# Kernel optimization log

Hardware: AMD Instinct MI355X
Metric: run time of the kernel (lower is better)

## Reference

```python
import jax, jax.numpy as jnp
import numpy as np

NB = 8            # num_blocks
D = 128           # embed_dim
D_INNER = 256     # expand=2
HEADS = 4
P = 64            # headdim
N = 32            # d_state
K = 4             # d_conv
CONV_DIM = D_INNER + 2 * N          # 320 (x, B, C streams)
D_IN_PROJ = 2 * D_INNER + 2 * N + HEADS  # 580 (z, xBC, dt)


def setup_inputs():
    key = jax.random.key(0)
    ks = iter(jax.random.split(key, 16))
    f = lambda shape, s=0.02: (jax.random.normal(next(ks), shape, jnp.float32) * s)
    B, L = 2, 4096
    return {
        'x': jax.random.normal(next(ks), (B, L, D), jnp.float32),
        'residual': jnp.zeros((B, L, D), jnp.float32),
        'ln1_w': jnp.ones((NB, D)), 'ln1_b': jnp.zeros((NB, D)),
        'ln2_w': jnp.ones((NB, D)), 'ln2_b': jnp.zeros((NB, D)),
        'fc1_w': f((NB, 4 * D, D)), 'fc1_b': jnp.zeros((NB, 4 * D)),
        'fc2_w': f((NB, D, 2 * D)), 'fc2_b': jnp.zeros((NB, D)),
        'in_proj_w': f((NB, D_IN_PROJ, D)),
        'conv_w': f((NB, CONV_DIM, K), 0.1), 'conv_b': jnp.zeros((NB, CONV_DIM)),
        'dt_bias': f((NB, HEADS), 0.1),
        'A_log': jnp.tile(jnp.log(jnp.arange(1, HEADS + 1, dtype=jnp.float32)), (NB, 1)),
        'Dp': jnp.ones((NB, HEADS)),
        'rms_w': jnp.ones((NB, D_INNER)),
        'out_proj_w': f((NB, D, D_INNER)),
        'h': 64, 'w': 64,
    }


def layernorm(x, w, b):
    mu = jnp.mean(x, -1, keepdims=True)
    var = jnp.mean((x - mu) ** 2, -1, keepdims=True)
    return (x - mu) * jax.lax.rsqrt(var + 1e-5) * w + b


def mamba2(x, in_proj_w, conv_w, conv_b, dt_bias, A_log, Dp, rms_w, out_proj_w):
    Bb, L, _ = x.shape
    zxbcdt = jnp.einsum('bld,ed->ble', x, in_proj_w)          # [B,L,580]
    z = zxbcdt[..., :D_INNER]
    xBC = zxbcdt[..., D_INNER:D_INNER + CONV_DIM]
    dt = jax.nn.softplus(zxbcdt[..., -HEADS:] + dt_bias)      # [B,L,H]
    # causal depthwise conv1d + silu
    xc = jnp.moveaxis(xBC, 1, 2)                              # [B,C,L]
    xc = jax.lax.conv_general_dilated(xc, conv_w[:, None, :], (1,), [(K - 1, 0)],
                                      feature_group_count=CONV_DIM)
    xBC = jax.nn.silu(jnp.moveaxis(xc, 1, 2) + conv_b)
    xs = xBC[..., :D_INNER].reshape(Bb, L, HEADS, P)          # [B,L,H,P]
    Bm = xBC[..., D_INNER:D_INNER + N]                        # [B,L,N]
    Cm = xBC[..., D_INNER + N:]                               # [B,L,N]
    dA = jnp.exp(dt * (-jnp.exp(A_log)))                      # [B,L,H]

    def step(hst, inp):
        dA_t, dt_t, B_t, C_t, x_t = inp
        hst = hst * dA_t[:, :, None, None] + (dt_t[:, :, None, None] * x_t[..., None]) * B_t[:, None, None, :]
        return hst, jnp.einsum('bhpn,bn->bhp', hst, C_t)

    tfirst = lambda a: jnp.moveaxis(a, 1, 0)
    h0 = jnp.zeros((Bb, HEADS, P, N), x.dtype)
    _, ys = jax.lax.scan(step, h0, (tfirst(dA), tfirst(dt), tfirst(Bm), tfirst(Cm), tfirst(xs)))
    y = jnp.moveaxis(ys, 0, 1) + Dp[None, None, :, None] * xs # [B,L,H,P]
    y = y.reshape(Bb, L, D_INNER) * jax.nn.silu(z)            # gated
    y = y * jax.lax.rsqrt(jnp.mean(y * y, -1, keepdims=True) + 1e-5) * rms_w
    return jnp.einsum('be,de->bd'.replace('b', 'bl'), y, out_proj_w)


def mlp(x, fc1_w, fc1_b, fc2_w, fc2_b):
    x12 = jnp.einsum('bld,ed->ble', x, fc1_w) + fc1_b
    x1, x2 = jnp.split(x12, 2, axis=-1)
    return jnp.einsum('ble,de->bld', jax.nn.silu(x1) * x2, fc2_w) + fc2_b


def reference(x, residual, ln1_w, ln1_b, ln2_w, ln2_b, fc1_w, fc1_b, fc2_w, fc2_b,
              in_proj_w, conv_w, conv_b, dt_bias, A_log, Dp, rms_w, out_proj_w, h, w):
    for i in range(NB):
        residual = x
        x1 = layernorm(residual, ln1_w[i], ln1_b[i])
        x_m = residual + mamba2(x1, in_proj_w[i], conv_w[i], conv_b[i], dt_bias[i],
                                A_log[i], Dp[i], rms_w[i], out_proj_w[i])
        residual = x_m
        x2 = layernorm(residual, ln2_w[i], ln2_b[i])
        x = residual + mlp(x2, fc1_w[i], fc1_b[i], fc2_w[i], fc2_b[i])
    return (x, residual)
```

## Files before the change

kernel.cpp:

```cpp
#include <hip/hip_runtime.h>
#include <hip/hip_bf16.h>
#include <cstddef>

#define NBLK 8
#define DD   128
#define DI   256
#define NH   4
#define PP   64
#define NNs  32
#define EE   580
#define BB   2
#define LLEN 4096
#define ML   (BB*LLEN)
#define SEGS 256
#define TT   16
#define GPAD 264

typedef unsigned short u16;
typedef short bf16x8 __attribute__((ext_vector_type(8)));
typedef float f32x4 __attribute__((ext_vector_type(4)));

__device__ __forceinline__ float siluf(float x){ return x / (1.f + expf(-x)); }
__device__ __forceinline__ float b2f(u16 u){ return __uint_as_float((unsigned)u << 16); }
__device__ __forceinline__ u16 f2b(float f){
    __hip_bfloat16 h = __float2bfloat16(f);
    return *reinterpret_cast<u16*>(&h);
}
__device__ __forceinline__ void ld8f(const u16* p, float* f){
    ushort4 a = *(const ushort4*)p;
    ushort4 b = *(const ushort4*)(p + 4);
    f[0]=b2f(a.x); f[1]=b2f(a.y); f[2]=b2f(a.z); f[3]=b2f(a.w);
    f[4]=b2f(b.x); f[5]=b2f(b.y); f[6]=b2f(b.z); f[7]=b2f(b.w);
}

#define IPW_N (NBLK*EE*DD)
#define OPW_N (NBLK*DD*DI)
#define F1W_N (NBLK*512*DD)
#define F2W_N (NBLK*DD*DI)
#define CVT_TOT (IPW_N+OPW_N+F1W_N+F2W_N)

__global__ __launch_bounds__(256) void cvt_weights(const float* __restrict__ ip,
                                                   const float* __restrict__ op,
                                                   const float* __restrict__ f1,
                                                   const float* __restrict__ f2,
                                                   const float* __restrict__ xin,
                                                   u16* __restrict__ dip,
                                                   u16* __restrict__ dop,
                                                   u16* __restrict__ df1,
                                                   u16* __restrict__ df2,
                                                   float* __restrict__ xout)
{
    int i = blockIdx.x * 256 + threadIdx.x;
    if (i < IPW_N)                          dip[i] = f2b(ip[i]);
    else if (i < IPW_N + OPW_N)             dop[i - IPW_N] = f2b(op[i - IPW_N]);
    else if (i < IPW_N + OPW_N + F1W_N)     df1[i - IPW_N - OPW_N] = f2b(f1[i - IPW_N - OPW_N]);
    else                                    df2[i - IPW_N - OPW_N - F1W_N] = f2b(f2[i - IPW_N - OPW_N - F1W_N]);
    if (i < ML * DD) xout[i] = xin[i];
}

__global__ __launch_bounds__(256) void inproj_ln_gemm(const float* __restrict__ X,
                                                      const float* __restrict__ lnw,
                                                      const float* __restrict__ lnb,
                                                      const u16* __restrict__ W,
                                                      u16* __restrict__ C)
{
    __shared__ __align__(16) u16 Ash[64*128];
    __shared__ __align__(16) u16 Wsh[64*128];
    __shared__ float red[64][8];
    const int tid = threadIdx.x;
    const int wave = tid >> 6, lane = tid & 63;
    const int l15 = lane & 15, quad = lane >> 4;
    const int bm = blockIdx.y * 64;
    const int lrow = tid >> 2, sub = tid & 3;

    const float* xr = X + (size_t)(bm + lrow) * DD + sub*32;
    float4 xv[8];
    float ps = 0.f, pq = 0.f;
#pragma unroll
    for (int i = 0; i < 8; i++) {
        xv[i] = *(const float4*)(xr + i*4);
        ps += xv[i].x + xv[i].y + xv[i].z + xv[i].w;
        pq += xv[i].x*xv[i].x + xv[i].y*xv[i].y + xv[i].z*xv[i].z + xv[i].w*xv[i].w;
    }
    red[lrow][sub] = ps; red[lrow][4+sub] = pq;
    __syncthreads();
    float s = red[lrow][0]+red[lrow][1]+red[lrow][2]+red[lrow][3];
    float q = red[lrow][4]+red[lrow][5]+red[lrow][6]+red[lrow][7];
    float mu = s * (1.f/DD);
    float rstd = rsqrtf(q*(1.f/DD) - mu*mu + 1e-5f);
#pragma unroll
    for (int i = 0; i < 4; i++) {
        float4 a0 = xv[2*i], a1 = xv[2*i+1];
        int c0 = sub*32 + i*8;
        u16 o[8];
        o[0] = f2b((a0.x-mu)*rstd*lnw[c0+0] + lnb[c0+0]);
        o[1] = f2b((a0.y-mu)*rstd*lnw[c0+1] + lnb[c0+1]);
        o[2] = f2b((a0.z-mu)*rstd*lnw[c0+2] + lnb[c0+2]);
        o[3] = f2b((a0.w-mu)*rstd*lnw[c0+3] + lnb[c0+3]);
        o[4] = f2b((a1.x-mu)*rstd*lnw[c0+4] + lnb[c0+4]);
        o[5] = f2b((a1.y-mu)*rstd*lnw[c0+5] + lnb[c0+5]);
        o[6] = f2b((a1.z-mu)*rstd*lnw[c0+6] + lnb[c0+6]);
        o[7] = f2b((a1.w-mu)*rstd*lnw[c0+7] + lnb[c0+7]);
        *(uint4*)&Ash[((size_t)(sub*4+i)*64 + lrow) * 8] = *(uint4*)o;
    }

#pragma unroll 1
    for (int t2 = 0; t2 < 2; t2++) {
        int bn = (blockIdx.x * 2 + t2) * 64;
        __syncthreads();
#pragma unroll
        for (int i = 0; i < 4; i++) {
            int k8 = sub + 4*i;
            uint4 wv = make_uint4(0u,0u,0u,0u);
            if (bn + lrow < EE)
                wv = *(const uint4*)(W + (size_t)(bn + lrow) * DD + k8*8);
            *(uint4*)&Wsh[((size_t)k8*64 + lrow) * 8] = wv;
        }
        __syncthreads();

        f32x4 acc[4];
#pragma unroll
        for (int nt = 0; nt < 4; nt++) acc[nt] = (f32x4){0.f,0.f,0.f,0.f};
#pragma unroll
        for (int kk = 0; kk < 4; kk++) {
            bf16x8 af = *(const bf16x8*)&Ash[(((kk*4 + quad)*64) + wave*16 + l15) * 8];
#pragma unroll
            for (int nt = 0; nt < 4; nt++) {
                bf16x8 bfv = *(const bf16x8*)&Wsh[(((kk*4 + quad)*64) + nt*16 + l15) * 8];
                acc[nt] = __builtin_amdgcn_mfma_f32_16x16x32_bf16(af, bfv, acc[nt], 0, 0, 0);
            }
        }
#pragma unroll
        for (int nt = 0; nt < 4; nt++) {
            int n = bn + nt*16 + l15;
            if (n < EE) {
#pragma unroll
                for (int r = 0; r < 4; r++) {
                    int m = bm + wave*16 + quad*4 + r;
                    C[(size_t)m * EE + n] = f2b(acc[nt][r]);
                }
            }
        }
    }
}

__global__ __launch_bounds__(256) void scan1(const u16* __restrict__ zx,
                                             const float* __restrict__ cw,
                                             const float* __restrict__ cb,
                                             const float* __restrict__ dt_bias,
                                             const float* __restrict__ A_log,
                                             u16* __restrict__ seg,
                                             float* __restrict__ segsum)
{
    __shared__ float Bsh[4][TT*NNs];
    __shared__ float dts[4][TT], das[4][TT];
    int wv = threadIdx.x >> 6;
    int p = threadIdx.x & 63;
    int sg = blockIdx.x % (SEGS/4);
    int bh = blockIdx.x / (SEGS/4);
    int h = bh % NH;
    int b = bh / NH;
    int s = sg*4 + wv;
    int l0 = s * TT;
    int row0 = b * LLEN + l0;

    float xr[TT+3];
    const u16* xcol = zx + (size_t)row0 * EE + 256 + h*64 + p;
#pragma unroll
    for (int r = 0; r < TT+3; r++) {
        int l = l0 - 3 + r;
        xr[r] = (l >= 0) ? b2f(xcol[(ptrdiff_t)(r-3) * EE]) : 0.f;
    }
    float4 wx = *(const float4*)(cw + (size_t)(h*64+p) * 4);
    float cbx = cb[h*64+p];

    if (p < NNs) {
        float br[TT+3];
        const u16* bcol = zx + (size_t)row0 * EE + 512 + p;
#pragma unroll
        for (int r = 0; r < TT+3; r++) {
            int l = l0 - 3 + r;
            br[r] = (l >= 0) ? b2f(bcol[(ptrdiff_t)(r-3) * EE]) : 0.f;
        }
        float4 wb = *(const float4*)(cw + (size_t)(256+p) * 4);
        float cbb = cb[256+p];
#pragma unroll
        for (int t = 0; t < TT; t++)
            Bsh[wv][t*NNs + p] = siluf(cbb + wb.x*br[t] + wb.y*br[t+1] + wb.z*br[t+2] + wb.w*br[t+3]);
    }
    if (p < TT) {
        float v = b2f(zx[(size_t)(row0+p)*EE + (EE-NH) + h]) + dt_bias[h];
        float dt = (v > 20.f) ? v : log1pf(expf(v));
        dts[wv][p] = dt;
        das[wv][p] = expf(-expf(A_log[h]) * dt);
    }
    __syncthreads();

    float hreg[NNs];
#pragma unroll
    for (int n = 0; n < NNs; n++) hreg[n] = 0.f;
    float sdt = 0.f;
#pragma unroll
    for (int t = 0; t < TT; t++) {
        float dA = das[wv][t];
        float dt = dts[wv][t];
        float xv = siluf(cbx + wx.x*xr[t] + wx.y*xr[t+1] + wx.z*xr[t+2] + wx.w*xr[t+3]);
        float dtx = dt * xv;
#pragma unroll
        for (int n4 = 0; n4 < 8; n4++) {
            float4 Bv = *(const float4*)&Bsh[wv][t*NNs + n4*4];
            hreg[n4*4+0] = fmaf(hreg[n4*4+0], dA, dtx * Bv.x);
            hreg[n4*4+1] = fmaf(hreg[n4*4+1], dA, dtx * Bv.y);
            hreg[n4*4+2] = fmaf(hreg[n4*4+2], dA, dtx * Bv.z);
            hreg[n4*4+3] = fmaf(hreg[n4*4+3], dA, dtx * Bv.w);
        }
        sdt += dt;
    }
    int bidg = bh * SEGS + s;
    u16* dst = seg + ((size_t)bidg * PP + p) * NNs;
#pragma unroll
    for (int n8 = 0; n8 < 4; n8++) {
        u16 ob[8];
#pragma unroll
        for (int j = 0; j < 8; j++) ob[j] = f2b(hreg[n8*8 + j]);
        *(uint4*)(dst + n8*8) = *(uint4*)ob;
    }
    if (p == 0) segsum[bidg] = sdt;
}

__global__ __launch_bounds__(256) void scan2(u16* __restrict__ seg,
                                             const float* __restrict__ segsum,
                                             const float* __restrict__ A_log)
{
    int bh = blockIdx.x >> 3;
    int chunk = blockIdx.x & 7;
    int h = bh % NH;
    int entry = chunk * 256 + threadIdx.x;
    float negA = -expf(A_log[h]);
    float hs = 0.f;
    const float* ss = segsum + bh * SEGS;
    u16* base = seg + (size_t)bh * SEGS * (PP * NNs) + entry;
    for (int j0 = 0; j0 < SEGS; j0 += 16) {
        float e[16], a[16];
#pragma unroll
        for (int k = 0; k < 16; k++) {
            a[k] = ss[j0 + k];
            e[k] = b2f(base[(size_t)(j0 + k) * (PP * NNs)]);
        }
#pragma unroll
        for (int k = 0; k < 16; k++) {
            float Aj = expf(negA * a[k]);
            base[(size_t)(j0 + k) * (PP * NNs)] = f2b(hs);
            hs = fmaf(Aj, hs, e[k]);
        }
    }
}

__global__ __launch_bounds__(256) void scan3(const u16* __restrict__ zx,
                                             const float* __restrict__ cw,
                                             const float* __restrict__ cb,
                                             const float* __restrict__ dt_bias,
                                             const float* __restrict__ A_log,
                                             const u16* __restrict__ seg,
                                             const float* __restrict__ Dp,
                                             u16* __restrict__ y)
{
    __shared__ float BCsh[4][TT*64];
    __shared__ float dts[4][TT], das[4][TT];
    int wv = threadIdx.x >> 6;
    int p = threadIdx.x & 63;
    int sg = blockIdx.x % (SEGS/4);
    int bh = blockIdx.x / (SEGS/4);
    int h = bh % NH;
    int b = bh / NH;
    int s = sg*4 + wv;
    int l0 = s * TT;
    int row0 = b * LLEN + l0;

    float xr[TT+3];
    const u16* xcol = zx + (size_t)row0 * EE + 256 + h*64 + p;
#pragma unroll
    for (int r = 0; r < TT+3; r++) {
        int l = l0 - 3 + r;
        xr[r] = (l >= 0) ? b2f(xcol[(ptrdiff_t)(r-3) * EE]) : 0.f;
    }
    float4 wx = *(const float4*)(cw + (size_t)(h*64+p) * 4);
    float cbx = cb[h*64+p];

    {
        float br[TT+3];
        const u16* bcol = zx + (size_t)row0 * EE + 512 + p;
#pragma unroll
        for (int r = 0; r < TT+3; r++) {
            int l = l0 - 3 + r;
            br[r] = (l >= 0) ? b2f(bcol[(ptrdiff_t)(r-3) * EE]) : 0.f;
        }
        float4 wb = *(const float4*)(cw + (size_t)(256+p) * 4);
        float cbb = cb[256+p];
#pragma unroll
        for (int t = 0; t < TT; t++)
            BCsh[wv][t*64 + p] = siluf(cbb + wb.x*br[t] + wb.y*br[t+1] + wb.z*br[t+2] + wb.w*br[t+3]);
    }
    if (p < TT) {
        float v = b2f(zx[(size_t)(row0+p)*EE + (EE-NH) + h]) + dt_bias[h];
        float dt = (v > 20.f) ? v : log1pf(expf(v));
        dts[wv][p] = dt;
        das[wv][p] = expf(-expf(A_log[h]) * dt);
    }

    float hreg[NNs];
    int bidg = bh * SEGS + s;
    const u16* src = seg + ((size_t)bidg * PP + p) * NNs;
#pragma unroll
    for (int n8 = 0; n8 < 4; n8++) {
        float f[8];
        ld8f(src + n8*8, f);
#pragma unroll
        for (int j = 0; j < 8; j++) hreg[n8*8 + j] = f[j];
    }
    float dp = Dp[h];
    __syncthreads();

#pragma unroll
    for (int t = 0; t < TT; t++) {
        float dA = das[wv][t];
        float dt = dts[wv][t];
        float xv = siluf(cbx + wx.x*xr[t] + wx.y*xr[t+1] + wx.z*xr[t+2] + wx.w*xr[t+3]);
        float dtx = dt * xv;
        float acc = 0.f;
#pragma unroll
        for (int n4 = 0; n4 < 8; n4++) {
            float4 Bv = *(const float4*)&BCsh[wv][t*64 + n4*4];
            float4 Cv = *(const float4*)&BCsh[wv][t*64 + 32 + n4*4];
            hreg[n4*4+0] = fmaf(hreg[n4*4+0], dA, dtx * Bv.x);
            hreg[n4*4+1] = fmaf(hreg[n4*4+1], dA, dtx * Bv.y);
            hreg[n4*4+2] = fmaf(hreg[n4*4+2], dA, dtx * Bv.z);
            hreg[n4*4+3] = fmaf(hreg[n4*4+3], dA, dtx * Bv.w);
            acc = fmaf(hreg[n4*4+0], Cv.x, acc);
            acc = fmaf(hreg[n4*4+1], Cv.y, acc);
            acc = fmaf(hreg[n4*4+2], Cv.z, acc);
            acc = fmaf(hreg[n4*4+3], Cv.w, acc);
        }
        y[(size_t)(row0 + t) * DI + h*PP + p] = f2b(acc + dp * xv);
    }
}

__global__ __launch_bounds__(256) void grms_outproj_gemm(const u16* __restrict__ Y,
                                                         const u16* __restrict__ Z,
                                                         const float* __restrict__ rmsw,
                                                         const u16* __restrict__ W,
                                                         const float* __restrict__ resid,
                                                         float* __restrict__ C)
{
    __shared__ __align__(16) u16 Ash[32*256];
    __shared__ __align__(16) u16 Wsh[64*256];
    __shared__ float red[32][8];
    __shared__ float rl[32];
    const int tid = threadIdx.x;
    const int wave = tid >> 6, lane = tid & 63;
    const int l15 = lane & 15, quad = lane >> 4;
    const int rt = wave & 1, nq = wave >> 1;
    const int bm = blockIdx.y * 32;
    const int bn = blockIdx.x * 64;

    {
        int wrow = tid >> 2, ksub = tid & 3;
#pragma unroll
        for (int i = 0; i < 8; i++) {
            int k8 = ksub + 4*i;
            uint4 wv = *(const uint4*)(W + (size_t)(bn + wrow) * DI + k8*8);
            *(uint4*)&Wsh[((size_t)k8*64 + wrow) * 8] = wv;
        }
    }

    int lrow = tid >> 3, sub = tid & 7;
    const u16* yr = Y + (size_t)(bm + lrow) * DI + sub*32;
    const u16* zr = Z + (size_t)(bm + lrow) * EE + sub*32;
    float pq = 0.f;
#pragma unroll
    for (int i = 0; i < 4; i++) {
        float yv[8], zv[8];
        ld8f(yr + i*8, yv);
        ld8f(zr + i*8, zv);
        int c0 = sub*32 + i*8;
        u16 o[8];
#pragma unroll
        for (int j = 0; j < 8; j++) {
            float g = yv[j] * siluf(zv[j]);
            pq += g*g;
            o[j] = f2b(g * rmsw[c0 + j]);
        }
        *(uint4*)&Ash[((size_t)(sub*4 + i)*32 + lrow) * 8] = *(uint4*)o;
    }
    red[lrow][sub] = pq;
    __syncthreads();
    if (sub == 0) {
        float qq = 0.f;
#pragma unroll
        for (int j = 0; j < 8; j++) qq += red[lrow][j];
        rl[lrow] = rsqrtf(qq * (1.f/DI) + 1e-5f);
    }
    __syncthreads();

    f32x4 acc[2];
    acc[0] = (f32x4){0.f,0.f,0.f,0.f};
    acc[1] = (f32x4){0.f,0.f,0.f,0.f};
#pragma unroll
    for (int kk = 0; kk < 8; kk++) {
        bf16x8 af = *(const bf16x8*)&Ash[(((kk*4 + quad)*32) + rt*16 + l15) * 8];
#pragma unroll
        for (int nt = 0; nt < 2; nt++) {
            bf16x8 bfv = *(const bf16x8*)&Wsh[(((kk*4 + quad)*64) + nq*32 + nt*16 + l15) * 8];
            acc[nt] = __builtin_amdgcn_mfma_f32_16x16x32_bf16(af, bfv, acc[nt], 0, 0, 0);
        }
    }
#pragma unroll
    for (int nt = 0; nt < 2; nt++) {
        int n = bn + nq*32 + nt*16 + l15;
#pragma unroll
        for (int r = 0; r < 4; r++) {
            int lm = rt*16 + quad*4 + r;
            int m = bm + lm;
            C[(size_t)m * DD + n] = acc[nt][r] * rl[lm] + resid[(size_t)m * DD + n];
        }
    }
}

__global__ __launch_bounds__(512) void mlp_fused(const float* __restrict__ Xm,
                                                 const float* __restrict__ lnw,
                                                 const float* __restrict__ lnb,
                                                 const u16* __restrict__ W1,
                                                 const float* __restrict__ b1,
                                                 const u16* __restrict__ W2,
                                                 const float* __restrict__ b2,
                                                 float* __restrict__ Out,
                                                 float* __restrict__ out2)
{
    __shared__ __align__(16) u16 Ash[32*128];
    __shared__ __align__(16) u16 Wsh[128*128];
    __shared__ __align__(16) u16 Gsh[32*GPAD];
    __shared__ float Xsh[32*132];
    __shared__ float red[32][32];
    const int tid = threadIdx.x;
    const int wv = tid >> 6, lane = tid & 63;
    const int l15 = lane & 15, quad = lane >> 4;
    const int mt = wv & 1, ng = wv >> 1;
    const int bm = blockIdx.x * 32;

    {
        int lrow = tid >> 4, sub = tid & 15;
        const float* xr = Xm + (size_t)(bm + lrow) * DD + sub*8;
        float4 x0 = *(const float4*)xr;
        float4 x1 = *(const float4*)(xr + 4);
        *(float4*)&Xsh[lrow*132 + sub*8]     = x0;
        *(float4*)&Xsh[lrow*132 + sub*8 + 4] = x1;
        float ps = x0.x+x0.y+x0.z+x0.w + x1.x+x1.y+x1.z+x1.w;
        float pq = x0.x*x0.x+x0.y*x0.y+x0.z*x0.z+x0.w*x0.w
                 + x1.x*x1.x+x1.y*x1.y+x1.z*x1.z+x1.w*x1.w;
        red[lrow][sub] = ps; red[lrow][16+sub] = pq;
        __syncthreads();
        float s = 0.f, q = 0.f;
#pragma unroll
        for (int j = 0; j < 16; j++) { s += red[lrow][j]; q += red[lrow][16+j]; }
        float mu = s * (1.f/DD);
        float rstd = rsqrtf(q*(1.f/DD) - mu*mu + 1e-5f);
        int c0 = sub*8;
        float xa[8] = {x0.x,x0.y,x0.z,x0.w,x1.x,x1.y,x1.z,x1.w};
        u16 o[8];
#pragma unroll
        for (int j = 0; j < 8; j++)
            o[j] = f2b((xa[j]-mu)*rstd*lnw[c0+j] + lnb[c0+j]);
        *(uint4*)&Ash[((size_t)sub*32 + lrow) * 8] = *(uint4*)o;
    }
    __syncthreads();

    bf16x8 afr[4];
#pragma unroll
    for (int kk = 0; kk < 4; kk++)
        afr[kk] = *(const bf16x8*)&Ash[(((kk*4 + quad)*32) + mt*16 + l15) * 8];

    for (int p = 0; p < 4; p++) {
        __syncthreads();
        {
            int wrow = tid >> 2, ksub = tid & 3;
            int r1 = (wrow < 64) ? (p*64 + wrow) : (256 + p*64 + wrow - 64);
#pragma unroll
            for (int i = 0; i < 4; i++) {
                int k8 = ksub + 4*i;
                uint4 wvv = *(const uint4*)(W1 + (size_t)r1 * DD + k8*8);
                *(uint4*)&Wsh[((size_t)k8*128 + wrow) * 8] = wvv;
            }
        }
        __syncthreads();
        f32x4 aa = (f32x4){0.f,0.f,0.f,0.f};
        f32x4 bb = (f32x4){0.f,0.f,0.f,0.f};
#pragma unroll
        for (int kk = 0; kk < 4; kk++) {
            bf16x8 b1v = *(const bf16x8*)&Wsh[(((kk*4 + quad)*128) + ng*16 + l15) * 8];
            bf16x8 b2v = *(const bf16x8*)&Wsh[(((kk*4 + quad)*128) + 64 + ng*16 + l15) * 8];
            aa = __builtin_amdgcn_mfma_f32_16x16x32_bf16(afr[kk], b1v, aa, 0, 0, 0);
            bb = __builtin_amdgcn_mfma_f32_16x16x32_bf16(afr[kk], b2v, bb, 0, 0, 0);
        }
        int n1 = p*64 + ng*16 + l15;
        float ba = b1[n1];
        float bbv = b1[256 + n1];
#pragma unroll
        for (int r = 0; r < 4; r++) {
            float a = aa[r] + ba;
            float bq = bb[r] + bbv;
            int m = mt*16 + quad*4 + r;
            Gsh[m*GPAD + n1] = f2b(siluf(a) * bq);
        }
    }

    f32x4 acc2[2];
    acc2[0] = (f32x4){0.f,0.f,0.f,0.f};
    acc2[1] = (f32x4){0.f,0.f,0.f,0.f};
    for (int kh = 0; kh < 2; kh++) {
        __syncthreads();
        {
            int wrow = tid >> 2, ksub = tid & 3;
#pragma unroll
            for (int i = 0; i < 4; i++) {
                int k8 = ksub + 4*i;
                uint4 wvv = *(const uint4*)(W2 + (size_t)wrow * DI + kh*128 + k8*8);
                *(uint4*)&Wsh[((size_t)k8*128 + wrow) * 8] = wvv;
            }
        }
        __syncthreads();
#pragma unroll
        for (int kk = 0; kk < 4; kk++) {
            bf16x8 af = *(const bf16x8*)&Gsh[(mt*16 + l15)*GPAD + kh*128 + kk*32 + quad*8];
#pragma unroll
            for (int nt = 0; nt < 2; nt++) {
                bf16x8 bfv = *(const bf16x8*)&Wsh[(((kk*4 + quad)*128) + ng*32 + nt*16 + l15) * 8];
                acc2[nt] = __builtin_amdgcn_mfma_f32_16x16x32_bf16(af, bfv, acc2[nt], 0, 0, 0);
            }
        }
    }
#pragma unroll
    for (int nt = 0; nt < 2; nt++) {
        int n = ng*32 + nt*16 + l15;
        float bv = b2[n];
#pragma unroll
        for (int r = 0; r < 4; r++) {
            int lm = mt*16 + quad*4 + r;
            int m = bm + lm;
            float xmv = Xsh[lm*132 + n];
            float v = acc2[nt][r] + bv + xmv;
            Out[(size_t)m * DD + n] = v;
            if (out2) {
                out2[(size_t)m * DD + n] = v;
                out2[(size_t)ML*DD + (size_t)m * DD + n] = xmv;
            }
        }
    }
}

extern "C" void kernel_launch(void* const* d_in, const int* in_sizes, int n_in,
                              void* d_out, int out_size, void* d_ws, size_t ws_size,
                              hipStream_t stream)
{
    (void)in_sizes; (void)n_in; (void)out_size; (void)ws_size;
    const float* x_in      = (const float*)d_in[0];
    const float* ln1_w     = (const float*)d_in[2];
    const float* ln1_b     = (const float*)d_in[3];
    const float* ln2_w     = (const float*)d_in[4];
    const float* ln2_b     = (const float*)d_in[5];
    const float* fc1_w     = (const float*)d_in[6];
    const float* fc1_b     = (const float*)d_in[7];
    const float* fc2_w     = (const float*)d_in[8];
    const float* fc2_b     = (const float*)d_in[9];
    const float* in_proj_w = (const float*)d_in[10];
    const float* conv_w    = (const float*)d_in[11];
    const float* conv_b    = (const float*)d_in[12];
    const float* dt_bias   = (const float*)d_in[13];
    const float* A_log     = (const float*)d_in[14];
    const float* Dp        = (const float*)d_in[15];
    const float* rms_w     = (const float*)d_in[16];
    const float* out_proj_w= (const float*)d_in[17];

    float* ws = (float*)d_ws;
    size_t o = 0;
    float* bufX    = ws + o; o += (size_t)ML * DD;
    float* bufXm   = ws + o; o += (size_t)ML * DD;
    float* bufSegA = ws + o; o += (size_t)BB * NH * SEGS;
    u16* bufSeg   = (u16*)(ws + o); o += (size_t)BB * NH * SEGS * PP * NNs / 2;
    u16* bufBigH  = (u16*)(ws + o); o += ((size_t)ML * EE + 1) / 2;
    u16* bufYH    = (u16*)(ws + o); o += (size_t)ML * DI / 2;
    u16* wIpH     = (u16*)(ws + o); o += (IPW_N + 1) / 2;
    u16* wOpH     = (u16*)(ws + o); o += (OPW_N + 1) / 2;
    u16* wF1H     = (u16*)(ws + o); o += (F1W_N + 1) / 2;
    u16* wF2H     = (u16*)(ws + o); o += (F2W_N + 1) / 2;

    cvt_weights<<<CVT_TOT/256, 256, 0, stream>>>(in_proj_w, out_proj_w, fc1_w, fc2_w,
                                                 x_in, wIpH, wOpH, wF1H, wF2H, bufX);

    for (int i = 0; i < NBLK; i++) {
        const float* ln1wi = ln1_w + i * DD;
        const float* ln1bi = ln1_b + i * DD;
        const float* ln2wi = ln2_w + i * DD;
        const float* ln2bi = ln2_b + i * DD;
        const float* cwi   = conv_w + (size_t)i * 320 * 4;
        const float* cbi   = conv_b + (size_t)i * 320;
        const float* dtbi  = dt_bias + i * NH;
        const float* ali   = A_log + i * NH;
        const float* dpi   = Dp + i * NH;
        const float* rwi   = rms_w + (size_t)i * DI;
        const float* f1bi  = fc1_b + (size_t)i * 512;
        const float* f2bi  = fc2_b + (size_t)i * DD;
        const u16* ipwi = wIpH + (size_t)i * EE * DD;
        const u16* opwi = wOpH + (size_t)i * DD * DI;
        const u16* f1wi = wF1H + (size_t)i * 512 * DD;
        const u16* f2wi = wF2H + (size_t)i * DD * DI;

        inproj_ln_gemm<<<dim3(5, ML/64), 256, 0, stream>>>(bufX, ln1wi, ln1bi, ipwi, bufBigH);
        scan1<<<BB*NH*(SEGS/4), 256, 0, stream>>>(bufBigH, cwi, cbi, dtbi, ali, bufSeg, bufSegA);
        scan2<<<BB*NH*8, 256, 0, stream>>>(bufSeg, bufSegA, ali);
        scan3<<<BB*NH*(SEGS/4), 256, 0, stream>>>(bufBigH, cwi, cbi, dtbi, ali, bufSeg, dpi, bufYH);
        grms_outproj_gemm<<<dim3(2, ML/32), 256, 0, stream>>>(bufYH, bufBigH, rwi, opwi,
                                                              bufX, bufXm);
        mlp_fused<<<ML/32, 512, 0, stream>>>(bufXm, ln2wi, ln2bi, f1wi, f1bi,
                                             f2wi, f2bi, bufX,
                                             (i == NBLK-1) ? (float*)d_out : nullptr);
    }
}
```

Before: 775.4 us.

## Fuse gated RMSNorm out-projection into the MLP kernel per row tile

Merges the gated-RMSNorm plus out_proj GEMM kernel with the LayerNorm plus MLP kernel into one 512-thread kernel per 32-row tile. The out_proj result plus residual stays in shared memory and feeds LN2 directly. This removes one launch per layer and the fp32 round trip of the intermediate activation through global memory. In exchange, each block now loops over the full out_proj weight in two halves, shared memory grows to about 70 KB, and the kernel writes bufX in place, which relies on every block reading only its own rows.

```diff
diff --git a/kernel.cpp b/kernel.cpp
--- a/kernel.cpp
+++ b/kernel.cpp
@@ -345,102 +345,27 @@
     }
 }
 
-__global__ __launch_bounds__(256) void grms_outproj_gemm(const u16* __restrict__ Y,
-                                                         const u16* __restrict__ Z,
-                                                         const float* __restrict__ rmsw,
-                                                         const u16* __restrict__ W,
-                                                         const float* __restrict__ resid,
-                                                         float* __restrict__ C)
+__global__ __launch_bounds__(512) void tail_fused(const u16* __restrict__ Y,
+                                                  const u16* __restrict__ Z,
+                                                  const float* __restrict__ rmsw,
+                                                  const u16* __restrict__ Wop,
+                                                  const float* __restrict__ X,
+                                                  const float* __restrict__ lnw,
+                                                  const float* __restrict__ lnb,
+                                                  const u16* __restrict__ W1,
+                                                  const float* __restrict__ b1,
+                                                  const u16* __restrict__ W2,
+                                                  const float* __restrict__ b2,
+                                                  float* __restrict__ Out,
+                                                  float* __restrict__ out2)
 {
-    __shared__ __align__(16) u16 Ash[32*256];
-    __shared__ __align__(16) u16 Wsh[64*256];
-    __shared__ float red[32][8];
-    __shared__ float rl[32];
-    const int tid = threadIdx.x;
-    const int wave = tid >> 6, lane = tid & 63;
-    const int l15 = lane & 15, quad = lane >> 4;
-    const int rt = wave & 1, nq = wave >> 1;
-    const int bm = blockIdx.y * 32;
-    const int bn = blockIdx.x * 64;
-
-    {
-        int wrow = tid >> 2, ksub = tid & 3;
-#pragma unroll
-        for (int i = 0; i < 8; i++) {
-            int k8 = ksub + 4*i;
-            uint4 wv = *(const uint4*)(W + (size_t)(bn + wrow) * DI + k8*8);
-            *(uint4*)&Wsh[((size_t)k8*64 + wrow) * 8] = wv;
-        }
-    }
-
-    int lrow = tid >> 3, sub = tid & 7;
-    const u16* yr = Y + (size_t)(bm + lrow) * DI + sub*32;
-    const u16* zr = Z + (size_t)(bm + lrow) * EE + sub*32;
-    float pq = 0.f;
-#pragma unroll
-    for (int i = 0; i < 4; i++) {
-        float yv[8], zv[8];
-        ld8f(yr + i*8, yv);
-        ld8f(zr + i*8, zv);
-        int c0 = sub*32 + i*8;
-        u16 o[8];
-#pragma unroll
-        for (int j = 0; j < 8; j++) {
-            float g = yv[j] * siluf(zv[j]);
-            pq += g*g;
-            o[j] = f2b(g * rmsw[c0 + j]);
-        }
-        *(uint4*)&Ash[((size_t)(sub*4 + i)*32 + lrow) * 8] = *(uint4*)o;
-    }
-    red[lrow][sub] = pq;
-    __syncthreads();
-    if (sub == 0) {
-        float qq = 0.f;
-#pragma unroll
-        for (int j = 0; j < 8; j++) qq += red[lrow][j];
-        rl[lrow] = rsqrtf(qq * (1.f/DI) + 1e-5f);
-    }
-    __syncthreads();
-
-    f32x4 acc[2];
-    acc[0] = (f32x4){0.f,0.f,0.f,0.f};
-    acc[1] = (f32x4){0.f,0.f,0.f,0.f};
-#pragma unroll
-    for (int kk = 0; kk < 8; kk++) {
-        bf16x8 af = *(const bf16x8*)&Ash[(((kk*4 + quad)*32) + rt*16 + l15) * 8];
-#pragma unroll
-        for (int nt = 0; nt < 2; nt++) {
-            bf16x8 bfv = *(const bf16x8*)&Wsh[(((kk*4 + quad)*64) + nq*32 + nt*16 + l15) * 8];
-            acc[nt] = __builtin_amdgcn_mfma_f32_16x16x32_bf16(af, bfv, acc[nt], 0, 0, 0);
-        }
-    }
-#pragma unroll
-    for (int nt = 0; nt < 2; nt++) {
-        int n = bn + nq*32 + nt*16 + l15;
-#pragma unroll
-        for (int r = 0; r < 4; r++) {
-            int lm = rt*16 + quad*4 + r;
-            int m = bm + lm;
-            C[(size_t)m * DD + n] = acc[nt][r] * rl[lm] + resid[(size_t)m * DD + n];
-        }
-    }
-}
-
-__global__ __launch_bounds__(512) void mlp_fused(const float* __restrict__ Xm,
-                                                 const float* __restrict__ lnw,
-                                                 const float* __restrict__ lnb,
-                                                 const u16* __restrict__ W1,
-                                                 const float* __restrict__ b1,
-                                                 const u16* __restrict__ W2,
-                                                 const float* __restrict__ b2,
-                                                 float* __restrict__ Out,
-                                                 float* __restrict__ out2)
-{
-    __shared__ __align__(16) u16 Ash[32*128];
-    __shared__ __align__(16) u16 Wsh[128*128];
-    __shared__ __align__(16) u16 Gsh[32*GPAD];
-    __shared__ float Xsh[32*132];
-    __shared__ float red[32][32];
+    __shared__ __align__(16) unsigned char smem[70784];
+    u16*   Wsh = (u16*)smem;
+    u16*   SH1 = (u16*)(smem + 32768);
+    float* Xsh = (float*)(smem + 49664);
+    float (*red)[32] = (float(*)[32])(smem + 66560);
+    float* rl  = (float*)(smem + 70656);
+
     const int tid = threadIdx.x;
     const int wv = tid >> 6, lane = tid & 63;
     const int l15 = lane & 15, quad = lane >> 4;
@@ -449,11 +374,67 @@
 
     {
         int lrow = tid >> 4, sub = tid & 15;
-        const float* xr = Xm + (size_t)(bm + lrow) * DD + sub*8;
-        float4 x0 = *(const float4*)xr;
-        float4 x1 = *(const float4*)(xr + 4);
-        *(float4*)&Xsh[lrow*132 + sub*8]     = x0;
-        *(float4*)&Xsh[lrow*132 + sub*8 + 4] = x1;
+        const u16* yr = Y + (size_t)(bm + lrow) * DI + sub*16;
+        const u16* zr = Z + (size_t)(bm + lrow) * EE + sub*16;
+        float pq = 0.f;
+#pragma unroll
+        for (int i = 0; i < 2; i++) {
+            float yv[8], zv[8];
+            ld8f(yr + i*8, yv);
+            ld8f(zr + i*8, zv);
+            int c0 = sub*16 + i*8;
+            u16 o[8];
+#pragma unroll
+            for (int j = 0; j < 8; j++) {
+                float g = yv[j] * siluf(zv[j]);
+                pq += g*g;
+                o[j] = f2b(g * rmsw[c0 + j]);
+            }
+            *(uint4*)&SH1[((size_t)(sub*2 + i)*32 + lrow) * 8] = *(uint4*)o;
+        }
+        red[lrow][sub] = pq;
+    }
+    __syncthreads();
+    if (tid < 32) {
+        float qq = 0.f;
+#pragma unroll
+        for (int j = 0; j < 16; j++) qq += red[tid][j];
+        rl[tid] = rsqrtf(qq * (1.f/DI) + 1e-5f);
+    }
+    __syncthreads();
+
+#pragma unroll 1
+    for (int nh = 0; nh < 2; nh++) {
+        {
+            int wrow = tid >> 3, ksub = tid & 7;
+#pragma unroll
+            for (int i = 0; i < 4; i++) {
+                int k8 = ksub + 8*i;
+                *(uint4*)&Wsh[((size_t)k8*64 + wrow) * 8] =
+                    *(const uint4*)(Wop + (size_t)(nh*64 + wrow) * DI + k8*8);
+            }
+        }
+        __syncthreads();
+        f32x4 acc = (f32x4){0.f,0.f,0.f,0.f};
+#pragma unroll
+        for (int kk = 0; kk < 8; kk++) {
+            bf16x8 af = *(const bf16x8*)&SH1[(((kk*4 + quad)*32) + mt*16 + l15) * 8];
+            bf16x8 bfv = *(const bf16x8*)&Wsh[(((kk*4 + quad)*64) + ng*16 + l15) * 8];
+            acc = __builtin_amdgcn_mfma_f32_16x16x32_bf16(af, bfv, acc, 0, 0, 0);
+        }
+        int n = nh*64 + ng*16 + l15;
+#pragma unroll
+        for (int r = 0; r < 4; r++) {
+            int lm = mt*16 + quad*4 + r;
+            Xsh[lm*132 + n] = acc[r] * rl[lm] + X[(size_t)(bm + lm) * DD + n];
+        }
+        __syncthreads();
+    }
+
+    {
+        int lrow = tid >> 4, sub = tid & 15;
+        float4 x0 = *(const float4*)&Xsh[lrow*132 + sub*8];
+        float4 x1 = *(const float4*)&Xsh[lrow*132 + sub*8 + 4];
         float ps = x0.x+x0.y+x0.z+x0.w + x1.x+x1.y+x1.z+x1.w;
         float pq = x0.x*x0.x+x0.y*x0.y+x0.z*x0.z+x0.w*x0.w
                  + x1.x*x1.x+x1.y*x1.y+x1.z*x1.z+x1.w*x1.w;
@@ -470,15 +451,16 @@
 #pragma unroll
         for (int j = 0; j < 8; j++)
             o[j] = f2b((xa[j]-mu)*rstd*lnw[c0+j] + lnb[c0+j]);
-        *(uint4*)&Ash[((size_t)sub*32 + lrow) * 8] = *(uint4*)o;
+        *(uint4*)&SH1[((size_t)sub*32 + lrow) * 8] = *(uint4*)o;
     }
     __syncthreads();
 
     bf16x8 afr[4];
 #pragma unroll
     for (int kk = 0; kk < 4; kk++)
-        afr[kk] = *(const bf16x8*)&Ash[(((kk*4 + quad)*32) + mt*16 + l15) * 8];
-
+        afr[kk] = *(const bf16x8*)&SH1[(((kk*4 + quad)*32) + mt*16 + l15) * 8];
+
+    u16* Gsh = SH1;
     for (int p = 0; p < 4; p++) {
         __syncthreads();
         {
@@ -583,7 +565,6 @@
     float* ws = (float*)d_ws;
     size_t o = 0;
     float* bufX    = ws + o; o += (size_t)ML * DD;
-    float* bufXm   = ws + o; o += (size_t)ML * DD;
     float* bufSegA = ws + o; o += (size_t)BB * NH * SEGS;
     u16* bufSeg   = (u16*)(ws + o); o += (size_t)BB * NH * SEGS * PP * NNs / 2;
     u16* bufBigH  = (u16*)(ws + o); o += ((size_t)ML * EE + 1) / 2;
@@ -618,10 +599,8 @@
         scan1<<<BB*NH*(SEGS/4), 256, 0, stream>>>(bufBigH, cwi, cbi, dtbi, ali, bufSeg, bufSegA);
         scan2<<<BB*NH*8, 256, 0, stream>>>(bufSeg, bufSegA, ali);
         scan3<<<BB*NH*(SEGS/4), 256, 0, stream>>>(bufBigH, cwi, cbi, dtbi, ali, bufSeg, dpi, bufYH);
-        grms_outproj_gemm<<<dim3(2, ML/32), 256, 0, stream>>>(bufYH, bufBigH, rwi, opwi,
-                                                              bufX, bufXm);
-        mlp_fused<<<ML/32, 512, 0, stream>>>(bufXm, ln2wi, ln2bi, f1wi, f1bi,
-                                             f2wi, f2bi, bufX,
-                                             (i == NBLK-1) ? (float*)d_out : nullptr);
-    }
-}
+        tail_fused<<<ML/32, 512, 0, stream>>>(bufYH, bufBigH, rwi, opwi, bufX,
+                                              ln2wi, ln2bi, f1wi, f1bi, f2wi, f2bi,
+                                              bufX, (i == NBLK-1) ? (float*)d_out : nullptr);
+    }
+}
```

After: 739.7 us. 4.6% less time.
